# Kernel tuning notes

Hardware: AMD Instinct MI355X
Metric: run time of the kernel (lower is better)

## Reference

```python
import jax, jax.numpy as jnp
import numpy as np

T, B, DIN, DH, DOUT = 512, 256, 128, 512, 128


def setup_inputs() -> dict:
    key = jax.random.key(0)
    k1, k2, k3, k4 = jax.random.split(key, 4)
    xs = jax.random.normal(k1, (T, B, DIN), dtype=jnp.float32)
    W1x = 0.1 * jax.random.normal(k2, (DIN, DH), dtype=jnp.float32)
    # random orthogonal init for the recurrent weight, as in the original
    q, _ = jnp.linalg.qr(jax.random.normal(k3, (DH, DH), dtype=jnp.float32))
    W1h = q.astype(jnp.float32)
    b1 = jnp.zeros([], dtype=jnp.float32)
    W2 = 0.1 * jax.random.normal(k4, (DH, DOUT), dtype=jnp.float32)
    b2 = jnp.zeros([], dtype=jnp.float32)
    return {"xs": xs, "W1x": W1x, "W1h": W1h, "b1": b1, "W2": W2, "b2": b2}


def reference(xs, W1x, W1h, b1, W2, b2):
    # Precompute all input projections in one big GEMM: [T, B, DH]
    xproj = jnp.einsum('tbi,ih->tbh', xs, W1x)
    h0 = jnp.zeros((xs.shape[1], W1h.shape[0]), dtype=xs.dtype)

    def step(h, xp):
        h_new = jnp.tanh(xp + h @ W1h + b1)
        return h_new, None

    h_final, _ = jax.lax.scan(step, h0, xproj)
    return h_final @ W2 + b2
```

## Files before the change

kernel.cpp:

```cpp
#include <hip/hip_runtime.h>

#define T_STEPS 512
#define BATCH   256
#define DIN     128
#define DH      512
#define DOUT    128
#define RGRP    16

typedef __attribute__((ext_vector_type(8))) short  short8;
typedef __attribute__((ext_vector_type(4))) float  floatx4;

union Pack8 { short8 s; unsigned short h[8]; };

__device__ __forceinline__ float bf2f(unsigned short u) {
    union { unsigned int i; float f; } v; v.i = ((unsigned int)u) << 16; return v.f;
}
__device__ __forceinline__ unsigned short f2bf(float f) {
    union { float f; unsigned int i; } v; v.f = f;
    unsigned int b = v.i;
    b += 0x7FFFu + ((b >> 16) & 1u);
    return (unsigned short)(b >> 16);
}
__device__ __forceinline__ float fast_tanh(float v) {
    float ex = __expf(v + v);
    return 1.f - 2.f / (ex + 1.f);
}

__global__ void pack_b_kernel(const float* __restrict__ W,
                              unsigned short* __restrict__ Wp, int K, int N) {
    int idx = blockIdx.x * blockDim.x + threadIdx.x;
    if (idx >= K * N) return;
    int k = idx / N, n = idx % N;
    int nt = n >> 4, kc = k >> 5, quad = (k >> 3) & 3, j = k & 7;
    int lane = quad * 16 + (n & 15);
    int KC = K >> 5;
    Wp[((size_t)(nt * KC + kc) * 64 + lane) * 8 + j] = f2bf(W[idx]);
}

__global__ __launch_bounds__(256) void xproj_kernel(
        const float* __restrict__ xs,
        const unsigned short* __restrict__ W1xp,
        unsigned short* __restrict__ xp) {
    const int tid  = threadIdx.x;
    const int lane = tid & 63;
    const int w    = tid >> 6;
    const int m    = lane & 15;
    const int q    = lane >> 4;
    const long row0 = (long)blockIdx.x * 16;

    short8 a[4];
#pragma unroll
    for (int kc = 0; kc < 4; ++kc) {
        const float* src = xs + (row0 + m) * DIN + kc * 32 + q * 8;
        Pack8 av;
#pragma unroll
        for (int j = 0; j < 8; ++j) av.h[j] = f2bf(src[j]);
        a[kc] = av.s;
    }

#pragma unroll
    for (int i = 0; i < 8; ++i) {
        const int nt = w * 8 + i;
        floatx4 acc = {0.f, 0.f, 0.f, 0.f};
#pragma unroll
        for (int kc = 0; kc < 4; ++kc) {
            short8 b = *(const short8*)(W1xp + ((size_t)(nt * 4 + kc) * 64 + lane) * 8);
            acc = __builtin_amdgcn_mfma_f32_16x16x32_bf16(a[kc], b, acc, 0, 0, 0);
        }
#pragma unroll
        for (int r = 0; r < 4; ++r)
            xp[(row0 + q * 4 + r) * DH + nt * 16 + m] = f2bf(acc[r]);
    }
}

template <int LKC>
__global__ __launch_bounds__(512, 2) void rnn_kernel(
        const unsigned short* __restrict__ xp,
        const unsigned short* __restrict__ W1hp,
        const float* __restrict__ b1p,
        const float* __restrict__ W2,
        const float* __restrict__ b2p,
        float* __restrict__ out) {
    extern __shared__ unsigned short smem[];
    unsigned short* Hb = smem;
    unsigned short* Wl = smem + 2 * 16 * 520;
#define HB(b, r, c) Hb[(b) * 8320 + (r) * 520 + (c)]

    const int tid  = threadIdx.x;
    const int lane = tid & 63;
    const int w    = tid >> 6;
    const int m    = lane & 15;
    const int q    = lane >> 4;
    const int rg   = blockIdx.x;
    const float b1 = b1p[0];

    short8 bfr[8][4];
#pragma unroll
    for (int kc = 0; kc < 8; ++kc)
#pragma unroll
        for (int i = 0; i < 4; ++i)
            bfr[kc][i] = *(const short8*)(W1hp +
                ((size_t)((4 * w + i) * 16 + kc) * 64 + lane) * 8);

    if (LKC > 0) {
        for (int c = tid; c < LKC * 2048; c += 512) {
            int j = c >> 11;
            int r = c & 2047;
            int nt = r >> 6, ln = r & 63;
            *(short8*)&Wl[(size_t)c * 8] =
                *(const short8*)(W1hp + ((size_t)(nt * 16 + 8 + j) * 64 + ln) * 8);
        }
    }

    for (int c = tid; c < 1024; c += 512) {
        int row = c >> 6, cc = c & 63;
        const unsigned short* src = xp + (size_t)(rg * 16 + row) * DH + cc * 8;
        Pack8 pk;
#pragma unroll
        for (int j = 0; j < 8; ++j) pk.h[j] = f2bf(fast_tanh(bf2f(src[j]) + b1));
        *(short8*)&HB(0, row, cc * 8) = pk.s;
    }
    __syncthreads();

    constexpr int KB = 8 + LKC;
    constexpr int NG = (8 - LKC + 1) / 2;

    int p = 0;
#pragma unroll 1
    for (int t = 1; t < T_STEPS; ++t) {
        short8 sb[2][2][4];
#pragma unroll
        for (int g = 0; g < 2 && g < NG; ++g)
#pragma unroll
            for (int c = 0; c < 2; ++c) {
                int kc = KB + 2 * g + c;
                if (kc < 16)
#pragma unroll
                    for (int i = 0; i < 4; ++i)
                        sb[g][c][i] = *(const short8*)(W1hp +
                            ((size_t)((4 * w + i) * 16 + kc) * 64 + lane) * 8);
            }

        unsigned short xv[4][4];
#pragma unroll
        for (int i = 0; i < 4; ++i)
#pragma unroll
            for (int r = 0; r < 4; ++r)
                xv[i][r] = xp[((size_t)t * BATCH + rg * 16 + q * 4 + r) * DH +
                              (4 * w + i) * 16 + m];

        floatx4 acc[4];
#pragma unroll
        for (int i = 0; i < 4; ++i) acc[i] = (floatx4){0.f, 0.f, 0.f, 0.f};

#pragma unroll
        for (int kc = 0; kc < 8; ++kc) {
            short8 a = *(const short8*)&HB(p, m, kc * 32 + q * 8);
#pragma unroll
            for (int i = 0; i < 4; ++i)
                acc[i] = __builtin_amdgcn_mfma_f32_16x16x32_bf16(a, bfr[kc][i], acc[i], 0, 0, 0);
        }

#pragma unroll
        for (int j = 0; j < LKC; ++j) {
            short8 a = *(const short8*)&HB(p, m, (8 + j) * 32 + q * 8);
#pragma unroll
            for (int i = 0; i < 4; ++i) {
                short8 b = *(const short8*)&Wl[((size_t)(j * 32 + 4 * w + i) * 64 + lane) * 8];
                acc[i] = __builtin_amdgcn_mfma_f32_16x16x32_bf16(a, b, acc[i], 0, 0, 0);
            }
        }

#pragma unroll
        for (int g = 0; g < NG; ++g) {
#pragma unroll
            for (int c = 0; c < 2; ++c) {
                int kc = KB + 2 * g + c;
                if (kc < 16) {
                    short8 a = *(const short8*)&HB(p, m, kc * 32 + q * 8);
#pragma unroll
                    for (int i = 0; i < 4; ++i)
                        acc[i] = __builtin_amdgcn_mfma_f32_16x16x32_bf16(a, sb[g & 1][c][i], acc[i], 0, 0, 0);
                }
            }
            if (g + 2 < NG) {
#pragma unroll
                for (int c = 0; c < 2; ++c) {
                    int kc = KB + 2 * (g + 2) + c;
                    if (kc < 16)
#pragma unroll
                        for (int i = 0; i < 4; ++i)
                            sb[g & 1][c][i] = *(const short8*)(W1hp +
                                ((size_t)((4 * w + i) * 16 + kc) * 64 + lane) * 8);
                }
            }
        }

#pragma unroll
        for (int i = 0; i < 4; ++i)
#pragma unroll
            for (int r = 0; r < 4; ++r) {
                float v = acc[i][r] + bf2f(xv[i][r]) + b1;
                HB(1 - p, q * 4 + r, (4 * w + i) * 16 + m) = f2bf(fast_tanh(v));
            }
        __syncthreads();
        p ^= 1;
    }

    const float b2 = b2p[0];
    floatx4 acc = {0.f, 0.f, 0.f, 0.f};
#pragma unroll
    for (int kc = 0; kc < 16; ++kc) {
        short8 av = *(const short8*)&HB(p, m, kc * 32 + q * 8);
        Pack8 bv;
#pragma unroll
        for (int j = 0; j < 8; ++j)
            bv.h[j] = f2bf(W2[(size_t)(kc * 32 + q * 8 + j) * DOUT + w * 16 + m]);
        acc = __builtin_amdgcn_mfma_f32_16x16x32_bf16(av, bv.s, acc, 0, 0, 0);
    }
#pragma unroll
    for (int r = 0; r < 4; ++r)
        out[(size_t)(rg * 16 + q * 4 + r) * DOUT + w * 16 + m] = acc[r] + b2;
#undef HB
}

extern "C" void kernel_launch(void* const* d_in, const int* in_sizes, int n_in,
                              void* d_out, int out_size, void* d_ws, size_t ws_size,
                              hipStream_t stream) {
    const float* xs  = (const float*)d_in[0];
    const float* W1x = (const float*)d_in[1];
    const float* W1h = (const float*)d_in[2];
    const float* b1  = (const float*)d_in[3];
    const float* W2  = (const float*)d_in[4];
    const float* b2  = (const float*)d_in[5];
    float* out = (float*)d_out;

    unsigned short* xp   = (unsigned short*)d_ws;
    unsigned short* w1hp = xp + (size_t)T_STEPS * BATCH * DH;
    unsigned short* w1xp = w1hp + (size_t)DH * DH;

    pack_b_kernel<<<(DH * DH + 255) / 256, 256, 0, stream>>>(W1h, w1hp, DH, DH);
    pack_b_kernel<<<(DIN * DH + 255) / 256, 256, 0, stream>>>(W1x, w1xp, DIN, DH);
    xproj_kernel<<<(T_STEPS * BATCH) / 16, 256, 0, stream>>>(xs, w1xp, xp);

    constexpr size_t SMEM_BIG   = 2 * 16 * 520 * 2 + 3 * 32 * 64 * 8 * 2;
    constexpr size_t SMEM_SMALL = 2 * 16 * 520 * 2;
    hipError_t e = hipFuncSetAttribute(
        reinterpret_cast<const void*>(&rnn_kernel<3>),
        hipFuncAttributeMaxDynamicSharedMemorySize, (int)SMEM_BIG);
    if (e == hipSuccess) {
        rnn_kernel<3><<<RGRP, 512, SMEM_BIG, stream>>>(xp, w1hp, b1, W2, b2, out);
    } else {
        rnn_kernel<0><<<RGRP, 512, SMEM_SMALL, stream>>>(xp, w1hp, b1, W2, b2, out);
    }
}
```

Measured before the change: 1.679 ms.

## Fold bias into xproj, fragment-order xproj layout, swizzled LDS, rebalance weight residency

The input projection now adds b1 and is stored in an MFMA-fragment-ordered layout, so each thread loads its per-step x values with two 16-byte loads instead of sixteen scalar gathers. The hidden-state LDS buffer is stored in A-fragment order with an XOR swizzle instead of padded rows, meant to reduce bank conflicts on reads and writes. The split of W1h k-chunks shifts to 10 in registers, 2 in LDS and 4 streamed from global, which raises register pressure to lower L2 traffic. The streamed chunks are issued before the register-resident MFMAs to hide their latency.

```diff
diff --git a/kernel.cpp b/kernel.cpp
--- a/kernel.cpp
+++ b/kernel.cpp
@@ -9,6 +9,7 @@
 
 typedef __attribute__((ext_vector_type(8))) short  short8;
 typedef __attribute__((ext_vector_type(4))) float  floatx4;
+typedef __attribute__((ext_vector_type(4))) unsigned short ushort4v;
 
 union Pack8 { short8 s; unsigned short h[8]; };
 
@@ -40,13 +41,15 @@
 __global__ __launch_bounds__(256) void xproj_kernel(
         const float* __restrict__ xs,
         const unsigned short* __restrict__ W1xp,
-        unsigned short* __restrict__ xp) {
+        const float* __restrict__ b1p,
+        unsigned short* __restrict__ xpe) {
     const int tid  = threadIdx.x;
     const int lane = tid & 63;
     const int w    = tid >> 6;
     const int m    = lane & 15;
     const int q    = lane >> 4;
     const long row0 = (long)blockIdx.x * 16;
+    const float b1 = b1p[0];
 
     short8 a[4];
 #pragma unroll
@@ -67,24 +70,24 @@
             short8 b = *(const short8*)(W1xp + ((size_t)(nt * 4 + kc) * 64 + lane) * 8);
             acc = __builtin_amdgcn_mfma_f32_16x16x32_bf16(a[kc], b, acc, 0, 0, 0);
         }
-#pragma unroll
-        for (int r = 0; r < 4; ++r)
-            xp[(row0 + q * 4 + r) * DH + nt * 16 + m] = f2bf(acc[r]);
+        ushort4v sv;
+#pragma unroll
+        for (int r = 0; r < 4; ++r) sv[r] = f2bf(acc[r] + b1);
+        *(ushort4v*)&xpe[((size_t)blockIdx.x * 512 +
+                          (size_t)(nt >> 2) * 64 + lane) * 16 + (nt & 3) * 4] = sv;
     }
 }
 
 template <int LKC>
-__global__ __launch_bounds__(512, 2) void rnn_kernel(
-        const unsigned short* __restrict__ xp,
-        const unsigned short* __restrict__ W1hp,
-        const float* __restrict__ b1p,
-        const float* __restrict__ W2,
-        const float* __restrict__ b2p,
-        float* __restrict__ out) {
+__global__ __launch_bounds__(512) __attribute__((amdgpu_waves_per_eu(2, 2)))
+void rnn_kernel(const unsigned short* __restrict__ xpe,
+                const unsigned short* __restrict__ W1hp,
+                const float* __restrict__ W2,
+                const float* __restrict__ b2p,
+                float* __restrict__ out) {
     extern __shared__ unsigned short smem[];
     unsigned short* Hb = smem;
-    unsigned short* Wl = smem + 2 * 16 * 520;
-#define HB(b, r, c) Hb[(b) * 8320 + (r) * 520 + (c)]
+    unsigned short* Wl = smem + 16384;
 
     const int tid  = threadIdx.x;
     const int lane = tid & 63;
@@ -92,11 +95,14 @@
     const int m    = lane & 15;
     const int q    = lane >> 4;
     const int rg   = blockIdx.x;
-    const float b1 = b1p[0];
-
-    short8 bfr[8][4];
-#pragma unroll
-    for (int kc = 0; kc < 8; ++kc)
+
+    constexpr int RKC  = 10;
+    constexpr int SKC0 = RKC + LKC;
+    constexpr int NS   = 16 - RKC - LKC;
+
+    short8 bfr[RKC][4];
+#pragma unroll
+    for (int kc = 0; kc < RKC; ++kc)
 #pragma unroll
         for (int i = 0; i < 4; ++i)
             bfr[kc][i] = *(const short8*)(W1hp +
@@ -105,65 +111,96 @@
     if (LKC > 0) {
         for (int c = tid; c < LKC * 2048; c += 512) {
             int j = c >> 11;
-            int r = c & 2047;
-            int nt = r >> 6, ln = r & 63;
+            int r2 = c & 2047;
+            int nt = r2 >> 6, ln = r2 & 63;
             *(short8*)&Wl[(size_t)c * 8] =
-                *(const short8*)(W1hp + ((size_t)(nt * 16 + 8 + j) * 64 + ln) * 8);
-        }
-    }
-
-    for (int c = tid; c < 1024; c += 512) {
-        int row = c >> 6, cc = c & 63;
-        const unsigned short* src = xp + (size_t)(rg * 16 + row) * DH + cc * 8;
-        Pack8 pk;
-#pragma unroll
-        for (int j = 0; j < 8; ++j) pk.h[j] = f2bf(fast_tanh(bf2f(src[j]) + b1));
-        *(short8*)&HB(0, row, cc * 8) = pk.s;
+                *(const short8*)(W1hp + ((size_t)(nt * 16 + RKC + j) * 64 + ln) * 8);
+        }
+    }
+
+    const int slot = lane ^ ((lane >> 4) << 2) ^ (((lane >> 3) & 1) << 1);
+    int roff = slot * 8;
+
+    int widx[4];
+#pragma unroll
+    for (int i = 0; i < 4; ++i) {
+        int kcp = 2 * w + (i >> 1);
+        int qp  = (2 * i + (m >> 3)) & 3;
+        int lp  = 4 * q + 16 * qp;
+        int sl  = lp ^ ((lp >> 4) << 2) ^ (((lp >> 3) & 1) << 1);
+        widx[i] = kcp * 512 + sl * 8 + (m & 7);
+    }
+
+    {
+        const unsigned short* xb =
+            xpe + ((size_t)rg * 512 + (size_t)w * 64 + lane) * 16;
+        Pack8 x0, x1;
+        x0.s = ((const short8*)xb)[0];
+        x1.s = ((const short8*)xb)[1];
+#pragma unroll
+        for (int i = 0; i < 4; ++i) {
+            Pack8 xh = (i < 2) ? x0 : x1;
+#pragma unroll
+            for (int r = 0; r < 4; ++r) {
+                float v = bf2f(xh.h[(i & 1) * 4 + r]);
+                Hb[widx[i] ^ (r << 3)] = f2bf(fast_tanh(v));
+            }
+            widx[i] ^= 8192;
+        }
     }
     __syncthreads();
 
-    constexpr int KB = 8 + LKC;
-    constexpr int NG = (8 - LKC + 1) / 2;
-
-    int p = 0;
 #pragma unroll 1
     for (int t = 1; t < T_STEPS; ++t) {
-        short8 sb[2][2][4];
-#pragma unroll
-        for (int g = 0; g < 2 && g < NG; ++g)
-#pragma unroll
-            for (int c = 0; c < 2; ++c) {
-                int kc = KB + 2 * g + c;
-                if (kc < 16)
-#pragma unroll
-                    for (int i = 0; i < 4; ++i)
-                        sb[g][c][i] = *(const short8*)(W1hp +
-                            ((size_t)((4 * w + i) * 16 + kc) * 64 + lane) * 8);
-            }
-
-        unsigned short xv[4][4];
-#pragma unroll
-        for (int i = 0; i < 4; ++i)
-#pragma unroll
-            for (int r = 0; r < 4; ++r)
-                xv[i][r] = xp[((size_t)t * BATCH + rg * 16 + q * 4 + r) * DH +
-                              (4 * w + i) * 16 + m];
+        asm volatile("" ::: "memory");
+
+        const unsigned short* hrd = Hb + roff;
+
+        short8 sb[2][4];
+#pragma unroll
+        for (int g = 0; g < 2; ++g)
+#pragma unroll
+            for (int i = 0; i < 4; ++i)
+                sb[g][i] = *(const short8*)(W1hp +
+                    ((size_t)((4 * w + i) * 16 + SKC0 + g) * 64 + lane) * 8);
+
+        Pack8 x0, x1;
+        {
+            const unsigned short* xb = xpe +
+                (((size_t)t * 16 + rg) * 512 + (size_t)w * 64 + lane) * 16;
+            x0.s = ((const short8*)xb)[0];
+            x1.s = ((const short8*)xb)[1];
+        }
 
         floatx4 acc[4];
 #pragma unroll
         for (int i = 0; i < 4; ++i) acc[i] = (floatx4){0.f, 0.f, 0.f, 0.f};
 
 #pragma unroll
-        for (int kc = 0; kc < 8; ++kc) {
-            short8 a = *(const short8*)&HB(p, m, kc * 32 + q * 8);
+        for (int kc = 0; kc < RKC; ++kc) {
+            short8 a = *(const short8*)&hrd[kc * 512];
 #pragma unroll
             for (int i = 0; i < 4; ++i)
                 acc[i] = __builtin_amdgcn_mfma_f32_16x16x32_bf16(a, bfr[kc][i], acc[i], 0, 0, 0);
         }
 
 #pragma unroll
+        for (int g = 0; g < 2; ++g) {
+            short8 a = *(const short8*)&hrd[(SKC0 + g) * 512];
+#pragma unroll
+            for (int i = 0; i < 4; ++i)
+                acc[i] = __builtin_amdgcn_mfma_f32_16x16x32_bf16(a, sb[g][i], acc[i], 0, 0, 0);
+            if (g + 2 < NS) {
+#pragma unroll
+                for (int i = 0; i < 4; ++i)
+                    sb[g][i] = *(const short8*)(W1hp +
+                        ((size_t)((4 * w + i) * 16 + SKC0 + g + 2) * 64 + lane) * 8);
+            }
+        }
+
+#pragma unroll
         for (int j = 0; j < LKC; ++j) {
-            short8 a = *(const short8*)&HB(p, m, (8 + j) * 32 + q * 8);
+            short8 a = *(const short8*)&hrd[(RKC + j) * 512];
 #pragma unroll
             for (int i = 0; i < 4; ++i) {
                 short8 b = *(const short8*)&Wl[((size_t)(j * 32 + 4 * w + i) * 64 + lane) * 8];
@@ -172,46 +209,38 @@
         }
 
 #pragma unroll
-        for (int g = 0; g < NG; ++g) {
-#pragma unroll
-            for (int c = 0; c < 2; ++c) {
-                int kc = KB + 2 * g + c;
-                if (kc < 16) {
-                    short8 a = *(const short8*)&HB(p, m, kc * 32 + q * 8);
-#pragma unroll
-                    for (int i = 0; i < 4; ++i)
-                        acc[i] = __builtin_amdgcn_mfma_f32_16x16x32_bf16(a, sb[g & 1][c][i], acc[i], 0, 0, 0);
-                }
-            }
-            if (g + 2 < NG) {
-#pragma unroll
-                for (int c = 0; c < 2; ++c) {
-                    int kc = KB + 2 * (g + 2) + c;
-                    if (kc < 16)
-#pragma unroll
-                        for (int i = 0; i < 4; ++i)
-                            sb[g & 1][c][i] = *(const short8*)(W1hp +
-                                ((size_t)((4 * w + i) * 16 + kc) * 64 + lane) * 8);
-                }
-            }
-        }
-
-#pragma unroll
-        for (int i = 0; i < 4; ++i)
+        for (int g = 2; g < NS; ++g) {
+            short8 a = *(const short8*)&hrd[(SKC0 + g) * 512];
+#pragma unroll
+            for (int i = 0; i < 4; ++i)
+                acc[i] = __builtin_amdgcn_mfma_f32_16x16x32_bf16(a, sb[g & 1][i], acc[i], 0, 0, 0);
+            if (g + 2 < NS) {
+#pragma unroll
+                for (int i = 0; i < 4; ++i)
+                    sb[g & 1][i] = *(const short8*)(W1hp +
+                        ((size_t)((4 * w + i) * 16 + SKC0 + g + 2) * 64 + lane) * 8);
+            }
+        }
+
+#pragma unroll
+        for (int i = 0; i < 4; ++i) {
+            Pack8 xh = (i < 2) ? x0 : x1;
 #pragma unroll
             for (int r = 0; r < 4; ++r) {
-                float v = acc[i][r] + bf2f(xv[i][r]) + b1;
-                HB(1 - p, q * 4 + r, (4 * w + i) * 16 + m) = f2bf(fast_tanh(v));
-            }
+                float v = acc[i][r] + bf2f(xh.h[(i & 1) * 4 + r]);
+                Hb[widx[i] ^ (r << 3)] = f2bf(fast_tanh(v));
+            }
+            widx[i] ^= 8192;
+        }
+        roff ^= 8192;
         __syncthreads();
-        p ^= 1;
     }
 
     const float b2 = b2p[0];
     floatx4 acc = {0.f, 0.f, 0.f, 0.f};
 #pragma unroll
     for (int kc = 0; kc < 16; ++kc) {
-        short8 av = *(const short8*)&HB(p, m, kc * 32 + q * 8);
+        short8 av = *(const short8*)&Hb[roff + kc * 512];
         Pack8 bv;
 #pragma unroll
         for (int j = 0; j < 8; ++j)
@@ -221,7 +250,6 @@
 #pragma unroll
     for (int r = 0; r < 4; ++r)
         out[(size_t)(rg * 16 + q * 4 + r) * DOUT + w * 16 + m] = acc[r] + b2;
-#undef HB
 }
 
 extern "C" void kernel_launch(void* const* d_in, const int* in_sizes, int n_in,
@@ -235,22 +263,22 @@
     const float* b2  = (const float*)d_in[5];
     float* out = (float*)d_out;
 
-    unsigned short* xp   = (unsigned short*)d_ws;
-    unsigned short* w1hp = xp + (size_t)T_STEPS * BATCH * DH;
+    unsigned short* xpe  = (unsigned short*)d_ws;
+    unsigned short* w1hp = xpe + (size_t)T_STEPS * BATCH * DH;
     unsigned short* w1xp = w1hp + (size_t)DH * DH;
 
     pack_b_kernel<<<(DH * DH + 255) / 256, 256, 0, stream>>>(W1h, w1hp, DH, DH);
     pack_b_kernel<<<(DIN * DH + 255) / 256, 256, 0, stream>>>(W1x, w1xp, DIN, DH);
-    xproj_kernel<<<(T_STEPS * BATCH) / 16, 256, 0, stream>>>(xs, w1xp, xp);
-
-    constexpr size_t SMEM_BIG   = 2 * 16 * 520 * 2 + 3 * 32 * 64 * 8 * 2;
-    constexpr size_t SMEM_SMALL = 2 * 16 * 520 * 2;
+    xproj_kernel<<<(T_STEPS * BATCH) / 16, 256, 0, stream>>>(xs, w1xp, b1, xpe);
+
+    constexpr size_t SMEM_BIG   = 32768 + 2 * 32768;
+    constexpr size_t SMEM_SMALL = 32768;
     hipError_t e = hipFuncSetAttribute(
-        reinterpret_cast<const void*>(&rnn_kernel<3>),
+        reinterpret_cast<const void*>(&rnn_kernel<2>),
         hipFuncAttributeMaxDynamicSharedMemorySize, (int)SMEM_BIG);
     if (e == hipSuccess) {
-        rnn_kernel<3><<<RGRP, 512, SMEM_BIG, stream>>>(xp, w1hp, b1, W2, b2, out);
+        rnn_kernel<2><<<RGRP, 512, SMEM_BIG, stream>>>(xpe, w1hp, W2, b2, out);
     } else {
-        rnn_kernel<0><<<RGRP, 512, SMEM_SMALL, stream>>>(xp, w1hp, b1, W2, b2, out);
-    }
-}
+        rnn_kernel<0><<<RGRP, 512, SMEM_SMALL, stream>>>(xpe, w1hp, W2, b2, out);
+    }
+}
```

New measurement: 1.684 ms. Within noise of the previous version (+0.3%).
